# Kernel optimization log

Hardware: AMD Instinct MI355X
Metric: run time of the kernel (lower is better)

The kernel has to match this reference:

```python
import jax, jax.numpy as jnp
import numpy as np

NEG_SLOPE = 0.2


def setup_inputs() -> dict:
    key = jax.random.key(0)
    ks = jax.random.split(key, 8)
    N, E, FIN, H, D, C = 50000, 1000000, 128, 4, 32, 16
    feat = jax.random.normal(ks[0], (N, FIN), dtype=jnp.float32)
    y = jax.random.normal(ks[1], (N, C), dtype=jnp.float32)
    src = jax.random.randint(ks[2], (E,), 0, N, dtype=jnp.int32)
    dst = jax.random.randint(ks[3], (E,), 0, N, dtype=jnp.int32)
    fc_w = jax.random.normal(ks[4], (FIN, H * D), dtype=jnp.float32) * 0.05
    attn_l = jax.random.normal(ks[5], (H, D), dtype=jnp.float32) * 0.1
    attn_r = jax.random.normal(ks[6], (H, D), dtype=jnp.float32) * 0.1
    bias = jnp.zeros((H * D,), dtype=jnp.float32)
    return dict(feat=feat, y=y, fc_w=fc_w, attn_l=attn_l, attn_r=attn_r,
                bias=bias, src=src, dst=dst)


def reference(feat, y, fc_w, attn_l, attn_r, bias, src, dst):
    N = feat.shape[0]
    H, D = attn_l.shape
    # shared projection (feat_src == feat_dst for a homogeneous graph)
    ft = (feat @ fc_w).reshape(N, H, D)            # (N, H, D)
    el = jnp.sum(ft * attn_l[None], axis=-1)       # (N, H)
    er = jnp.sum(ft * attn_r[None], axis=-1)       # (N, H)
    # per-edge score: e_ij = leaky_relu(el[src] + er[dst])
    e = jax.nn.leaky_relu(el[src] + er[dst], negative_slope=NEG_SLOPE)  # (E, H)
    # segment softmax over edges grouped by destination node
    m = jax.ops.segment_max(e, dst, num_segments=N)                     # (N, H)
    m = jnp.where(jnp.isfinite(m), m, jnp.zeros_like(m))                # empty segments
    ee = jnp.exp(e - m[dst])                                            # (E, H)
    s = jax.ops.segment_sum(ee, dst, num_segments=N)                    # (N, H)
    a = ee / jnp.maximum(s[dst], 1e-9)                                  # (E, H)
    # scatter-aggregate weighted messages
    msg = ft[src] * a[:, :, None]                                       # (E, H, D)
    rst = jax.ops.segment_sum(msg, dst, num_segments=N)                 # (N, H, D)
    rst = rst + bias.reshape(1, H, D)
    # propagate labels y with the same attention (broadcast (C,) * (H,1) -> (H,C))
    ymsg = y[src][:, None, :] * a[:, :, None]                           # (E, H, C)
    y_pred = jax.ops.segment_sum(ymsg, dst, num_segments=N)             # (N, H, C)
    return rst, y_pred
```

## Files before the change

kernel.cpp:

```cpp
#include <hip/hip_runtime.h>
#include <hip/hip_bf16.h>

#define NEG_SLOPE 0.2f
#define ROWB 320
#define BSLOT 96
#define NSUBMAX 256
#define QCAP2 64
#define SUBSHIFT 8
#define SUBCAP 6400

typedef unsigned short u16;
typedef unsigned int u32;
typedef unsigned long long u64;

__device__ __forceinline__ u16 f32_to_bf16(float x) {
    u32 u = __float_as_uint(x);
    u32 r = u + 0x7fffu + ((u >> 16) & 1u);
    return (u16)(r >> 16);
}
__device__ __forceinline__ u32 bf16pair(float a, float b) {
    return (u32)f32_to_bf16(a) | ((u32)f32_to_bf16(b) << 16);
}
__device__ __forceinline__ float bflo(u32 u) { return __uint_as_float(u << 16); }
__device__ __forceinline__ float bfhi(u32 u) { return __uint_as_float(u & 0xffff0000u); }

__global__ __launch_bounds__(256) void k_binA2(
    const int* __restrict__ src, const int* __restrict__ dst,
    u32* __restrict__ subQ, int* __restrict__ subCursor, int nSub, int E) {
    __shared__ u32 q[NSUBMAX * QCAP2];
    __shared__ int lcnt[NSUBMAX], lbase[NSUBMAX];
    int t = threadIdx.x;
    lcnt[t] = 0;
    __syncthreads();
    int base = blockIdx.x * 4096;
#define PUSH(dd, sv)                                                      \
    {                                                                     \
        u32 bin_ = (u32)(dd) >> SUBSHIFT;                                 \
        u32 pair_ = ((u32)(dd) << 16) | ((u32)(sv) & 0xffffu);            \
        int p_ = atomicAdd(&lcnt[bin_], 1);                               \
        if (p_ < QCAP2) q[bin_ * QCAP2 + p_] = pair_;                     \
        else {                                                            \
            int gp_ = atomicAdd(&subCursor[bin_], 1);                     \
            if (gp_ < SUBCAP) subQ[(size_t)bin_ * SUBCAP + gp_] = pair_;  \
        }                                                                 \
    }
    for (int it = 0; it < 4; ++it) {
        int i = base + it * 1024 + t * 4;
        if (i + 4 <= E) {
            int4 d = *(const int4*)(dst + i);
            int4 s = *(const int4*)(src + i);
            PUSH(d.x, s.x); PUSH(d.y, s.y); PUSH(d.z, s.z); PUSH(d.w, s.w);
        } else {
            for (int k = 0; k < 4 && i + k < E; ++k) PUSH(dst[i + k], src[i + k]);
        }
    }
#undef PUSH
    __syncthreads();
    if (t < nSub) {
        int c = min(lcnt[t], QCAP2);
        lbase[t] = atomicAdd(&subCursor[t], c);
    }
    __syncthreads();
    int lane = t & 63, wv = t >> 6;
    for (int b = wv; b < nSub; b += 4) {
        int c = min(lcnt[b], QCAP2);
        if (lane < c) {
            int gp = lbase[b] + lane;
            if (gp < SUBCAP) subQ[(size_t)b * SUBCAP + gp] = q[b * QCAP2 + lane];
        }
    }
}

__global__ __launch_bounds__(256) void k_fused(
    const float* __restrict__ feat, const float* __restrict__ fc_w,
    const float* __restrict__ y, const float* __restrict__ attn_l,
    const float* __restrict__ attn_r, char* __restrict__ comb,
    const u32* __restrict__ subQ, const int* __restrict__ subCursor,
    int* __restrict__ cnt, u16* __restrict__ ss, int N, int nSub) {
    __shared__ u32 w_lds[128 * 64];
    __shared__ float f_lds[64 * 128];
    int t = threadIdx.x;

    if ((int)blockIdx.x < nSub) {
        int b = blockIdx.x;
        int* hist = (int*)w_lds;
        int* cur = hist + 256;
        hist[t] = 0;
        cur[t] = 0;
        __syncthreads();
        int n_b = min(subCursor[b], SUBCAP);
        const u32* qb = subQ + (size_t)b * SUBCAP;

        for (int i = t * 4; i < n_b; i += 1024) {
            if (i + 4 <= n_b) {
                uint4 p4 = *(const uint4*)(qb + i);
                atomicAdd(&hist[(p4.x >> 16) & 255], 1);
                atomicAdd(&hist[(p4.y >> 16) & 255], 1);
                atomicAdd(&hist[(p4.z >> 16) & 255], 1);
                atomicAdd(&hist[(p4.w >> 16) & 255], 1);
            } else {
                for (int k = i; k < n_b; ++k) atomicAdd(&hist[(qb[k] >> 16) & 255], 1);
            }
        }
        __syncthreads();
        int node = (b << SUBSHIFT) + t;
        if (node < N) cnt[node] = min(hist[t], BSLOT);

        for (int i = t * 4; i < n_b; i += 1024) {
            if (i + 4 <= n_b) {
                uint4 p4 = *(const uint4*)(qb + i);
                u32 pa[4] = {p4.x, p4.y, p4.z, p4.w};
#pragma unroll
                for (int k = 0; k < 4; ++k) {
                    int r = (pa[k] >> 16) & 255;
                    int p = atomicAdd(&cur[r], 1);
                    if (p < BSLOT)
                        ss[(size_t)(pa[k] >> 16) * BSLOT + p] = (u16)(pa[k] & 0xffffu);
                }
            } else {
                for (int k = i; k < n_b; ++k) {
                    u32 pr = qb[k];
                    int r = (pr >> 16) & 255;
                    int p = atomicAdd(&cur[r], 1);
                    if (p < BSLOT)
                        ss[(size_t)(pr >> 16) * BSLOT + p] = (u16)(pr & 0xffffu);
                }
            }
        }
        return;
    }

    int pb = (int)blockIdx.x - nSub;
    int n0 = pb * 64;
    if (pb == 0 && t < 80) {
        float* srow = (float*)(comb + (size_t)N * ROWB);
        srow[t] = (t >= 72 && t < 76) ? -1e30f : 0.f;
    }

#pragma unroll
    for (int it = 0; it < 16; ++it) {
        int i = it * 256 + t;
        float4 v = *(const float4*)(fc_w + 4 * i);
        int k = i >> 5, cp = 2 * (i & 31);
        *(uint2*)(w_lds + k * 64 + cp) = make_uint2(bf16pair(v.x, v.y), bf16pair(v.z, v.w));
    }
#pragma unroll
    for (int it = 0; it < 8; ++it) {
        int i = it * 256 + t;
        int n = i >> 5, q4 = 4 * (i & 31);
        float4 v = make_float4(0.f, 0.f, 0.f, 0.f);
        if (n0 + n < N) v = *(const float4*)(feat + (size_t)(n0 + n) * 128 + q4);
        *(float4*)(f_lds + n * 128 + q4) = v;
    }
#pragma unroll
    for (int it = 0; it < 4; ++it) {
        int i = it * 256 + t;
        int n = i >> 4, col = i & 15;
        if (n0 + n < N) {
            float yv = y[(size_t)(n0 + n) * 16 + col];
            *(u16*)(comb + (size_t)(n0 + n) * ROWB + 256 + 2 * col) = f32_to_bf16(yv);
        }
    }
    __syncthreads();

    int c = t & 31;
    int g = t >> 5;

    float acc[8][4];
#pragma unroll
    for (int j = 0; j < 8; ++j)
#pragma unroll
        for (int q = 0; q < 4; ++q) acc[j][q] = 0.f;

    const u32* wp = w_lds + 2 * c;
    const float* fp = f_lds + (8 * g) * 128;
    for (int k = 0; k < 128; k += 4) {
        uint2 wq0 = *(const uint2*)(wp + (k + 0) * 64);
        uint2 wq1 = *(const uint2*)(wp + (k + 1) * 64);
        uint2 wq2 = *(const uint2*)(wp + (k + 2) * 64);
        uint2 wq3 = *(const uint2*)(wp + (k + 3) * 64);
        float w00 = bflo(wq0.x), w01 = bfhi(wq0.x), w02 = bflo(wq0.y), w03 = bfhi(wq0.y);
        float w10 = bflo(wq1.x), w11 = bfhi(wq1.x), w12 = bflo(wq1.y), w13 = bfhi(wq1.y);
        float w20 = bflo(wq2.x), w21 = bfhi(wq2.x), w22 = bflo(wq2.y), w23 = bfhi(wq2.y);
        float w30 = bflo(wq3.x), w31 = bfhi(wq3.x), w32 = bflo(wq3.y), w33 = bfhi(wq3.y);
#pragma unroll
        for (int j = 0; j < 8; ++j) {
            float4 f = *(const float4*)(fp + j * 128 + k);
            acc[j][0] = fmaf(f.x, w00, acc[j][0]);
            acc[j][1] = fmaf(f.x, w01, acc[j][1]);
            acc[j][2] = fmaf(f.x, w02, acc[j][2]);
            acc[j][3] = fmaf(f.x, w03, acc[j][3]);
            acc[j][0] = fmaf(f.y, w10, acc[j][0]);
            acc[j][1] = fmaf(f.y, w11, acc[j][1]);
            acc[j][2] = fmaf(f.y, w12, acc[j][2]);
            acc[j][3] = fmaf(f.y, w13, acc[j][3]);
            acc[j][0] = fmaf(f.z, w20, acc[j][0]);
            acc[j][1] = fmaf(f.z, w21, acc[j][1]);
            acc[j][2] = fmaf(f.z, w22, acc[j][2]);
            acc[j][3] = fmaf(f.z, w23, acc[j][3]);
            acc[j][0] = fmaf(f.w, w30, acc[j][0]);
            acc[j][1] = fmaf(f.w, w31, acc[j][1]);
            acc[j][2] = fmaf(f.w, w32, acc[j][2]);
            acc[j][3] = fmaf(f.w, w33, acc[j][3]);
        }
    }

    float4 al4 = *(const float4*)(attn_l + 4 * c);
    float4 ar4 = *(const float4*)(attn_r + 4 * c);

#pragma unroll
    for (int j = 0; j < 8; ++j) {
        int n = n0 + 8 * g + j;
        bool ok = n < N;
        char* row = comb + (size_t)n * ROWB;
        if (ok) {
            *(uint2*)(row + 8 * c) =
                make_uint2(bf16pair(acc[j][0], acc[j][1]), bf16pair(acc[j][2], acc[j][3]));
        }
        float p = acc[j][0] * al4.x + acc[j][1] * al4.y + acc[j][2] * al4.z + acc[j][3] * al4.w;
        float q = acc[j][0] * ar4.x + acc[j][1] * ar4.y + acc[j][2] * ar4.z + acc[j][3] * ar4.w;
#pragma unroll
        for (int off = 1; off < 8; off <<= 1) {
            p += __shfl_xor(p, off);
            q += __shfl_xor(q, off);
        }
        if (ok && (c & 7) == 0) {
            float* ep = (float*)(row + 288);
            ep[c >> 3] = p;
            ep[4 + (c >> 3)] = q;
        }
    }
}

__global__ __launch_bounds__(256) void k_agg(
    const char* __restrict__ comb, const float* __restrict__ bias,
    const int* __restrict__ cnt, const u16* __restrict__ ss,
    float* __restrict__ rst, float* __restrict__ yp, int N) {
    __shared__ float ee_lds[4][256];
    int w = (int)((blockIdx.x * (size_t)blockDim.x + threadIdx.x) >> 6);
    int lane = threadIdx.x & 63;
    int wv = threadIdx.x >> 6;
    if (w >= N) return;

    int sub = lane & 31;
    int p = lane >> 5;
    bool isft = sub < 16;
    bool isy = (sub >= 16) && (sub < 24);
    int head = isft ? (sub >> 2) : (isy ? ((sub - 16) >> 1) : 0);
    int voff = isft ? 16 * sub : (256 + 16 * ((sub - 16) & 1));

    const char* roww = comb + (size_t)w * ROWB;
    float4 er4 = *(const float4*)(roww + 304);

    int deg = min(cnt[w], BSLOT);
    int degp = min((deg + 7) & ~7, BSLOT);
    int beg = w * BSLOT;

    float acc0 = 0.f, acc1 = 0.f, acc2 = 0.f, acc3 = 0.f;
    float acc4 = 0.f, acc5 = 0.f, acc6 = 0.f, acc7 = 0.f;
    float ssum = 0.f;
    float* my_ee = &ee_lds[wv][0];
    const float* eeL = my_ee + 4 * p + head;

#define LOADS(qq, V, Ee)                                        \
    {                                                           \
        int s0_ = __builtin_amdgcn_readlane(my_s, 2 * (qq));    \
        int s1_ = __builtin_amdgcn_readlane(my_s, 2 * (qq) + 1);\
        int s_ = p ? s1_ : s0_;                                 \
        const char* rb_ = comb + (size_t)s_ * ROWB;             \
        V = *(const uint4*)(rb_ + voff);                        \
        Ee = eeL[8 * (qq)];                                     \
    }
#define COMPS(V, Ee)                                            \
    {                                                           \
        ssum += Ee;                                             \
        acc0 = fmaf(Ee, bflo(V.x), acc0);                       \
        acc1 = fmaf(Ee, bfhi(V.x), acc1);                       \
        acc2 = fmaf(Ee, bflo(V.y), acc2);                       \
        acc3 = fmaf(Ee, bfhi(V.y), acc3);                       \
        acc4 = fmaf(Ee, bflo(V.z), acc4);                       \
        acc5 = fmaf(Ee, bfhi(V.z), acc5);                       \
        acc6 = fmaf(Ee, bflo(V.w), acc6);                       \
        acc7 = fmaf(Ee, bfhi(V.w), acc7);                       \
    }
#define LOAD4A(gg)                                              \
    {                                                           \
        int b4_ = 4 * (gg);                                     \
        LOADS(b4_ + 0, va0, ea0); LOADS(b4_ + 1, va1, ea1);     \
        LOADS(b4_ + 2, va2, ea2); LOADS(b4_ + 3, va3, ea3);     \
    }
#define LOAD4B(gg)                                              \
    {                                                           \
        int b4_ = 4 * (gg);                                     \
        LOADS(b4_ + 0, vb0, eb0); LOADS(b4_ + 1, vb1, eb1);     \
        LOADS(b4_ + 2, vb2, eb2); LOADS(b4_ + 3, vb3, eb3);     \
    }
#define COMP4A { COMPS(va0, ea0); COMPS(va1, ea1); COMPS(va2, ea2); COMPS(va3, ea3); }
#define COMP4B { COMPS(vb0, eb0); COMPS(vb1, eb1); COMPS(vb2, eb2); COMPS(vb3, eb3); }

    for (int off = 0; off < degp; off += 64) {
        int cl = min(64, degp - off);
        int my_s = (int)ss[beg + off + lane];
        my_s = (off + lane < deg) ? my_s : N;

        {
            const float4 el4 = *(const float4*)(comb + (size_t)my_s * ROWB + 288);
            float4 e4;
            e4.x = el4.x + er4.x;
            e4.y = el4.y + er4.y;
            e4.z = el4.z + er4.z;
            e4.w = el4.w + er4.w;
            float4 ee4;
            ee4.x = __expf(fmaxf(e4.x, NEG_SLOPE * e4.x));
            ee4.y = __expf(fmaxf(e4.y, NEG_SLOPE * e4.y));
            ee4.z = __expf(fmaxf(e4.z, NEG_SLOPE * e4.z));
            ee4.w = __expf(fmaxf(e4.w, NEG_SLOPE * e4.w));
            *(float4*)(my_ee + 4 * lane) = ee4;
        }

        int ngr = cl >> 3;
        uint4 va0, va1, va2, va3, vb0, vb1, vb2, vb3;
        float ea0, ea1, ea2, ea3, eb0, eb1, eb2, eb3;

        LOAD4A(0);
        int q = 0;
        for (; q + 2 <= ngr; q += 2) {
            LOAD4B(q + 1);
            COMP4A;
            if (q + 2 < ngr) LOAD4A(q + 2);
            COMP4B;
        }
        if (q < ngr) COMP4A;
    }
#undef LOADS
#undef COMPS
#undef LOAD4A
#undef LOAD4B
#undef COMP4A
#undef COMP4B

    ssum += __shfl_xor(ssum, 32);
    acc0 += __shfl_xor(acc0, 32);
    acc1 += __shfl_xor(acc1, 32);
    acc2 += __shfl_xor(acc2, 32);
    acc3 += __shfl_xor(acc3, 32);
    acc4 += __shfl_xor(acc4, 32);
    acc5 += __shfl_xor(acc5, 32);
    acc6 += __shfl_xor(acc6, 32);
    acc7 += __shfl_xor(acc7, 32);

    float inv = 1.f / fmaxf(ssum, 1e-9f);
    if (p == 0) {
        if (isft) {
            float4 b0 = *(const float4*)(bias + 8 * sub);
            float4 b1 = *(const float4*)(bias + 8 * sub + 4);
            float4 o0 = make_float4(fmaf(acc0, inv, b0.x), fmaf(acc1, inv, b0.y),
                                    fmaf(acc2, inv, b0.z), fmaf(acc3, inv, b0.w));
            float4 o1 = make_float4(fmaf(acc4, inv, b1.x), fmaf(acc5, inv, b1.y),
                                    fmaf(acc6, inv, b1.z), fmaf(acc7, inv, b1.w));
            *(float4*)(rst + (size_t)w * 128 + 8 * sub) = o0;
            *(float4*)(rst + (size_t)w * 128 + 8 * sub + 4) = o1;
        } else if (isy) {
            int yi = sub - 16;
            int hh = yi >> 1, hf = yi & 1;
            float4 o0 = make_float4(acc0 * inv, acc1 * inv, acc2 * inv, acc3 * inv);
            float4 o1 = make_float4(acc4 * inv, acc5 * inv, acc6 * inv, acc7 * inv);
            *(float4*)(yp + (size_t)w * 64 + 16 * hh + 8 * hf) = o0;
            *(float4*)(yp + (size_t)w * 64 + 16 * hh + 8 * hf + 4) = o1;
        }
    }
}

extern "C" void kernel_launch(void* const* d_in, const int* in_sizes, int n_in,
                              void* d_out, int out_size, void* d_ws, size_t ws_size,
                              hipStream_t stream) {
    const float* feat   = (const float*)d_in[0];
    const float* y      = (const float*)d_in[1];
    const float* fc_w   = (const float*)d_in[2];
    const float* attn_l = (const float*)d_in[3];
    const float* attn_r = (const float*)d_in[4];
    const float* bias   = (const float*)d_in[5];
    const int*   src    = (const int*)d_in[6];
    const int*   dst    = (const int*)d_in[7];

    const int N = in_sizes[0] / 128;
    const int E = in_sizes[6];

    char* comb = (char*)d_ws;
    int* cnt = (int*)(comb + (size_t)(N + 1) * ROWB);
    int* subCursor = cnt + N;
    u16* ss = (u16*)(subCursor + NSUBMAX);
    u32* subQ = (u32*)(ss + (size_t)BSLOT * N);

    float* rst = (float*)d_out;
    float* yp = rst + (size_t)N * 128;

    const int nSub = (N + 255) >> SUBSHIFT;
    const int projB = (N + 63) / 64;
    const int binAB = (E + 4095) / 4096;

    (void)hipMemsetAsync(subCursor, 0, NSUBMAX * sizeof(int), stream);
    k_binA2<<<dim3(binAB), dim3(256), 0, stream>>>(
        src, dst, subQ, subCursor, nSub, E);
    k_fused<<<dim3(nSub + projB), dim3(256), 0, stream>>>(
        feat, fc_w, y, attn_l, attn_r, comb, subQ, subCursor, cnt, ss, N, nSub);
    k_agg<<<dim3(((size_t)N * 64 + 255) / 256), dim3(256), 0, stream>>>(
        comb, bias, cnt, ss, rst, yp, N);
}
```

Measured before the change: 120.4 us.

## Fuse edge binning with projection and move per-node bucketing into separate kernel

The first binning pass (edge to sub-bin queues) now runs inside the same launch as the feature projection, reusing the projection's shared-memory buffers as the per-bin staging queue. The second pass (per-node histogram and slot scatter) moves out of the fused kernel into its own kernel. The aim is to overlap the atomic-heavy binning with the compute-bound projection instead of running binning alone. The cost is a heavier block mix in one launch and an extra launch for the per-node pass.

New measurement: 123.6 us. +2.7%, slower.

```diff
diff --git a/kernel.cpp b/kernel.cpp
--- a/kernel.cpp
+++ b/kernel.cpp
@@ -24,113 +24,67 @@
 __device__ __forceinline__ float bflo(u32 u) { return __uint_as_float(u << 16); }
 __device__ __forceinline__ float bfhi(u32 u) { return __uint_as_float(u & 0xffff0000u); }
 
-__global__ __launch_bounds__(256) void k_binA2(
-    const int* __restrict__ src, const int* __restrict__ dst,
-    u32* __restrict__ subQ, int* __restrict__ subCursor, int nSub, int E) {
-    __shared__ u32 q[NSUBMAX * QCAP2];
-    __shared__ int lcnt[NSUBMAX], lbase[NSUBMAX];
-    int t = threadIdx.x;
-    lcnt[t] = 0;
-    __syncthreads();
-    int base = blockIdx.x * 4096;
-#define PUSH(dd, sv)                                                      \
-    {                                                                     \
-        u32 bin_ = (u32)(dd) >> SUBSHIFT;                                 \
-        u32 pair_ = ((u32)(dd) << 16) | ((u32)(sv) & 0xffffu);            \
-        int p_ = atomicAdd(&lcnt[bin_], 1);                               \
-        if (p_ < QCAP2) q[bin_ * QCAP2 + p_] = pair_;                     \
-        else {                                                            \
-            int gp_ = atomicAdd(&subCursor[bin_], 1);                     \
-            if (gp_ < SUBCAP) subQ[(size_t)bin_ * SUBCAP + gp_] = pair_;  \
-        }                                                                 \
-    }
-    for (int it = 0; it < 4; ++it) {
-        int i = base + it * 1024 + t * 4;
-        if (i + 4 <= E) {
-            int4 d = *(const int4*)(dst + i);
-            int4 s = *(const int4*)(src + i);
-            PUSH(d.x, s.x); PUSH(d.y, s.y); PUSH(d.z, s.z); PUSH(d.w, s.w);
-        } else {
-            for (int k = 0; k < 4 && i + k < E; ++k) PUSH(dst[i + k], src[i + k]);
-        }
-    }
-#undef PUSH
-    __syncthreads();
-    if (t < nSub) {
-        int c = min(lcnt[t], QCAP2);
-        lbase[t] = atomicAdd(&subCursor[t], c);
-    }
-    __syncthreads();
-    int lane = t & 63, wv = t >> 6;
-    for (int b = wv; b < nSub; b += 4) {
-        int c = min(lcnt[b], QCAP2);
-        if (lane < c) {
-            int gp = lbase[b] + lane;
-            if (gp < SUBCAP) subQ[(size_t)b * SUBCAP + gp] = q[b * QCAP2 + lane];
-        }
-    }
-}
-
-__global__ __launch_bounds__(256) void k_fused(
+__global__ __launch_bounds__(256) void k_f1(
     const float* __restrict__ feat, const float* __restrict__ fc_w,
     const float* __restrict__ y, const float* __restrict__ attn_l,
     const float* __restrict__ attn_r, char* __restrict__ comb,
-    const u32* __restrict__ subQ, const int* __restrict__ subCursor,
-    int* __restrict__ cnt, u16* __restrict__ ss, int N, int nSub) {
+    const int* __restrict__ src, const int* __restrict__ dst,
+    u32* __restrict__ subQ, int* __restrict__ subCursor,
+    int N, int E, int nSub, int binAB) {
     __shared__ u32 w_lds[128 * 64];
     __shared__ float f_lds[64 * 128];
+    __shared__ int aux[512];
     int t = threadIdx.x;
 
-    if ((int)blockIdx.x < nSub) {
-        int b = blockIdx.x;
-        int* hist = (int*)w_lds;
-        int* cur = hist + 256;
-        hist[t] = 0;
-        cur[t] = 0;
+    if ((int)blockIdx.x < binAB) {
+        int* lcnt = aux;
+        int* lbase = aux + 256;
+        lcnt[t] = 0;
         __syncthreads();
-        int n_b = min(subCursor[b], SUBCAP);
-        const u32* qb = subQ + (size_t)b * SUBCAP;
-
-        for (int i = t * 4; i < n_b; i += 1024) {
-            if (i + 4 <= n_b) {
-                uint4 p4 = *(const uint4*)(qb + i);
-                atomicAdd(&hist[(p4.x >> 16) & 255], 1);
-                atomicAdd(&hist[(p4.y >> 16) & 255], 1);
-                atomicAdd(&hist[(p4.z >> 16) & 255], 1);
-                atomicAdd(&hist[(p4.w >> 16) & 255], 1);
+        int base = blockIdx.x * 4096;
+#define PUSH(dd, sv)                                                      \
+        {                                                                 \
+            u32 bin_ = (u32)(dd) >> SUBSHIFT;                             \
+            u32 pair_ = ((u32)(dd) << 16) | ((u32)(sv) & 0xffffu);        \
+            int p_ = atomicAdd(&lcnt[bin_], 1);                           \
+            if (p_ < QCAP2) {                                             \
+                u32* q_ = (bin_ & 128u) ? (u32*)f_lds : w_lds;            \
+                q_[(bin_ & 127u) * QCAP2 + p_] = pair_;                   \
+            } else {                                                      \
+                int gp_ = atomicAdd(&subCursor[bin_], 1);                 \
+                if (gp_ < SUBCAP) subQ[(size_t)bin_ * SUBCAP + gp_] = pair_; \
+            }                                                             \
+        }
+        for (int it = 0; it < 4; ++it) {
+            int i = base + it * 1024 + t * 4;
+            if (i + 4 <= E) {
+                int4 d = *(const int4*)(dst + i);
+                int4 s = *(const int4*)(src + i);
+                PUSH(d.x, s.x); PUSH(d.y, s.y); PUSH(d.z, s.z); PUSH(d.w, s.w);
             } else {
-                for (int k = i; k < n_b; ++k) atomicAdd(&hist[(qb[k] >> 16) & 255], 1);
+                for (int k = 0; k < 4 && i + k < E; ++k) PUSH(dst[i + k], src[i + k]);
             }
         }
+#undef PUSH
         __syncthreads();
-        int node = (b << SUBSHIFT) + t;
-        if (node < N) cnt[node] = min(hist[t], BSLOT);
-
-        for (int i = t * 4; i < n_b; i += 1024) {
-            if (i + 4 <= n_b) {
-                uint4 p4 = *(const uint4*)(qb + i);
-                u32 pa[4] = {p4.x, p4.y, p4.z, p4.w};
-#pragma unroll
-                for (int k = 0; k < 4; ++k) {
-                    int r = (pa[k] >> 16) & 255;
-                    int p = atomicAdd(&cur[r], 1);
-                    if (p < BSLOT)
-                        ss[(size_t)(pa[k] >> 16) * BSLOT + p] = (u16)(pa[k] & 0xffffu);
-                }
-            } else {
-                for (int k = i; k < n_b; ++k) {
-                    u32 pr = qb[k];
-                    int r = (pr >> 16) & 255;
-                    int p = atomicAdd(&cur[r], 1);
-                    if (p < BSLOT)
-                        ss[(size_t)(pr >> 16) * BSLOT + p] = (u16)(pr & 0xffffu);
-                }
+        if (t < nSub) {
+            int c = min(lcnt[t], QCAP2);
+            lbase[t] = atomicAdd(&subCursor[t], c);
+        }
+        __syncthreads();
+        int lane = t & 63, wv = t >> 6;
+        for (int b = wv; b < nSub; b += 4) {
+            int c = min(lcnt[b], QCAP2);
+            if (lane < c) {
+                int gp = lbase[b] + lane;
+                const u32* q_ = (b & 128) ? (const u32*)f_lds : w_lds;
+                if (gp < SUBCAP) subQ[(size_t)b * SUBCAP + gp] = q_[(b & 127) * QCAP2 + lane];
             }
         }
         return;
     }
 
-    int pb = (int)blockIdx.x - nSub;
+    int pb = (int)blockIdx.x - binAB;
     int n0 = pb * 64;
     if (pb == 0 && t < 80) {
         float* srow = (float*)(comb + (size_t)N * ROWB);
@@ -232,6 +186,57 @@
     }
 }
 
+__global__ __launch_bounds__(256) void k_passC(
+    const u32* __restrict__ subQ, const int* __restrict__ subCursor,
+    int* __restrict__ cnt, u16* __restrict__ ss, int N) {
+    __shared__ int hist[256];
+    __shared__ int cur[256];
+    int t = threadIdx.x;
+    int b = blockIdx.x;
+    hist[t] = 0;
+    cur[t] = 0;
+    __syncthreads();
+    int n_b = min(subCursor[b], SUBCAP);
+    const u32* qb = subQ + (size_t)b * SUBCAP;
+
+    for (int i = t * 4; i < n_b; i += 1024) {
+        if (i + 4 <= n_b) {
+            uint4 p4 = *(const uint4*)(qb + i);
+            atomicAdd(&hist[(p4.x >> 16) & 255], 1);
+            atomicAdd(&hist[(p4.y >> 16) & 255], 1);
+            atomicAdd(&hist[(p4.z >> 16) & 255], 1);
+            atomicAdd(&hist[(p4.w >> 16) & 255], 1);
+        } else {
+            for (int k = i; k < n_b; ++k) atomicAdd(&hist[(qb[k] >> 16) & 255], 1);
+        }
+    }
+    __syncthreads();
+    int node = (b << SUBSHIFT) + t;
+    if (node < N) cnt[node] = min(hist[t], BSLOT);
+
+    for (int i = t * 4; i < n_b; i += 1024) {
+        if (i + 4 <= n_b) {
+            uint4 p4 = *(const uint4*)(qb + i);
+            u32 pa[4] = {p4.x, p4.y, p4.z, p4.w};
+#pragma unroll
+            for (int k = 0; k < 4; ++k) {
+                int r = (pa[k] >> 16) & 255;
+                int p = atomicAdd(&cur[r], 1);
+                if (p < BSLOT)
+                    ss[(size_t)(pa[k] >> 16) * BSLOT + p] = (u16)(pa[k] & 0xffffu);
+            }
+        } else {
+            for (int k = i; k < n_b; ++k) {
+                u32 pr = qb[k];
+                int r = (pr >> 16) & 255;
+                int p = atomicAdd(&cur[r], 1);
+                if (p < BSLOT)
+                    ss[(size_t)(pr >> 16) * BSLOT + p] = (u16)(pr & 0xffffu);
+            }
+        }
+    }
+}
+
 __global__ __launch_bounds__(256) void k_agg(
     const char* __restrict__ comb, const float* __restrict__ bias,
     const int* __restrict__ cnt, const u16* __restrict__ ss,
@@ -400,10 +405,10 @@
     const int binAB = (E + 4095) / 4096;
 
     (void)hipMemsetAsync(subCursor, 0, NSUBMAX * sizeof(int), stream);
-    k_binA2<<<dim3(binAB), dim3(256), 0, stream>>>(
-        src, dst, subQ, subCursor, nSub, E);
-    k_fused<<<dim3(nSub + projB), dim3(256), 0, stream>>>(
-        feat, fc_w, y, attn_l, attn_r, comb, subQ, subCursor, cnt, ss, N, nSub);
+    k_f1<<<dim3(binAB + projB), dim3(256), 0, stream>>>(
+        feat, fc_w, y, attn_l, attn_r, comb, src, dst, subQ, subCursor,
+        N, E, nSub, binAB);
+    k_passC<<<dim3(nSub), dim3(256), 0, stream>>>(subQ, subCursor, cnt, ss, N);
     k_agg<<<dim3(((size_t)N * 64 + 255) / 256), dim3(256), 0, stream>>>(
         comb, bias, cnt, ss, rst, yp, N);
 }
```

## Compute node projection GEMM with bf16 MFMA instead of scalar FMAs

Applied to the files above, without the earlier changes.

Replaces the scalar-FMA feat@fc_w projection in the fused kernel with __builtin_amdgcn_mfma_f32_16x16x32_bf16. Weights and features are staged in LDS as bf16 in an MFMA-friendly layout, with padded feature rows to reduce bank conflicts. Results go back through LDS so the existing epilogue can compute el/er and write rows. This adds an extra LDS round trip and barrier, and el/er are now computed from bf16-rounded features, a small precision change.

Result: faster. 109.0 us (median of 3 runs) (-9.5%).

```diff
diff --git a/kernel.cpp b/kernel.cpp
--- a/kernel.cpp
+++ b/kernel.cpp
@@ -12,6 +12,8 @@
 typedef unsigned short u16;
 typedef unsigned int u32;
 typedef unsigned long long u64;
+typedef __attribute__((ext_vector_type(8))) short bf16x8;
+typedef __attribute__((ext_vector_type(4))) float f32x4;
 
 __device__ __forceinline__ u16 f32_to_bf16(float x) {
     u32 u = __float_as_uint(x);
@@ -77,14 +79,14 @@
     const float* __restrict__ attn_r, char* __restrict__ comb,
     const u32* __restrict__ subQ, const int* __restrict__ subCursor,
     int* __restrict__ cnt, u16* __restrict__ ss, int N, int nSub) {
-    __shared__ u32 w_lds[128 * 64];
-    __shared__ float f_lds[64 * 128];
+    __shared__ u16 w16[16384];
+    __shared__ u16 f16[64 * 136];
+    __shared__ int hist[256];
+    __shared__ int cur[256];
     int t = threadIdx.x;
 
     if ((int)blockIdx.x < nSub) {
         int b = blockIdx.x;
-        int* hist = (int*)w_lds;
-        int* cur = hist + 256;
         hist[t] = 0;
         cur[t] = 0;
         __syncthreads();
@@ -141,16 +143,22 @@
     for (int it = 0; it < 16; ++it) {
         int i = it * 256 + t;
         float4 v = *(const float4*)(fc_w + 4 * i);
-        int k = i >> 5, cp = 2 * (i & 31);
-        *(uint2*)(w_lds + k * 64 + cp) = make_uint2(bf16pair(v.x, v.y), bf16pair(v.z, v.w));
+        int k = i >> 5, jq = i & 31;
+        int kt = k >> 5, h2 = (k >> 3) & 3, i0 = k & 7;
+        int jt = jq >> 2, jm0 = (jq & 3) * 4;
+        int base = ((jt * 4 + kt) * 64 + 16 * h2 + jm0) * 8 + i0;
+        w16[base] = f32_to_bf16(v.x);
+        w16[base + 8] = f32_to_bf16(v.y);
+        w16[base + 16] = f32_to_bf16(v.z);
+        w16[base + 24] = f32_to_bf16(v.w);
     }
 #pragma unroll
     for (int it = 0; it < 8; ++it) {
         int i = it * 256 + t;
-        int n = i >> 5, q4 = 4 * (i & 31);
+        int n = i >> 5, q4 = (i & 31) * 4;
         float4 v = make_float4(0.f, 0.f, 0.f, 0.f);
         if (n0 + n < N) v = *(const float4*)(feat + (size_t)(n0 + n) * 128 + q4);
-        *(float4*)(f_lds + n * 128 + q4) = v;
+        *(uint2*)(f16 + n * 136 + q4) = make_uint2(bf16pair(v.x, v.y), bf16pair(v.z, v.w));
     }
 #pragma unroll
     for (int it = 0; it < 4; ++it) {
@@ -163,48 +171,35 @@
     }
     __syncthreads();
 
+    int wv2 = t >> 6, l = t & 63;
+    int m = l & 15, h = l >> 4;
+
+    f32x4 acc[8];
+#pragma unroll
+    for (int jt = 0; jt < 8; ++jt) acc[jt] = (f32x4){0.f, 0.f, 0.f, 0.f};
+
+    const u16* arow = f16 + (16 * wv2 + m) * 136 + 8 * h;
+#pragma unroll
+    for (int kt = 0; kt < 4; ++kt) {
+        uint4 av = *(const uint4*)(arow + kt * 32);
+        bf16x8 a = __builtin_bit_cast(bf16x8, av);
+#pragma unroll
+        for (int jt = 0; jt < 8; ++jt) {
+            uint4 bv = *(const uint4*)(w16 + ((jt * 4 + kt) * 64 + l) * 8);
+            bf16x8 bfr = __builtin_bit_cast(bf16x8, bv);
+            acc[jt] = __builtin_amdgcn_mfma_f32_16x16x32_bf16(a, bfr, acc[jt], 0, 0, 0);
+        }
+    }
+
+#pragma unroll
+    for (int jt = 0; jt < 8; ++jt)
+#pragma unroll
+        for (int r = 0; r < 4; ++r)
+            f16[(16 * wv2 + 4 * h + r) * 136 + 16 * jt + m] = f32_to_bf16(acc[jt][r]);
+    __syncthreads();
+
     int c = t & 31;
     int g = t >> 5;
-
-    float acc[8][4];
-#pragma unroll
-    for (int j = 0; j < 8; ++j)
-#pragma unroll
-        for (int q = 0; q < 4; ++q) acc[j][q] = 0.f;
-
-    const u32* wp = w_lds + 2 * c;
-    const float* fp = f_lds + (8 * g) * 128;
-    for (int k = 0; k < 128; k += 4) {
-        uint2 wq0 = *(const uint2*)(wp + (k + 0) * 64);
-        uint2 wq1 = *(const uint2*)(wp + (k + 1) * 64);
-        uint2 wq2 = *(const uint2*)(wp + (k + 2) * 64);
-        uint2 wq3 = *(const uint2*)(wp + (k + 3) * 64);
-        float w00 = bflo(wq0.x), w01 = bfhi(wq0.x), w02 = bflo(wq0.y), w03 = bfhi(wq0.y);
-        float w10 = bflo(wq1.x), w11 = bfhi(wq1.x), w12 = bflo(wq1.y), w13 = bfhi(wq1.y);
-        float w20 = bflo(wq2.x), w21 = bfhi(wq2.x), w22 = bflo(wq2.y), w23 = bfhi(wq2.y);
-        float w30 = bflo(wq3.x), w31 = bfhi(wq3.x), w32 = bflo(wq3.y), w33 = bfhi(wq3.y);
-#pragma unroll
-        for (int j = 0; j < 8; ++j) {
-            float4 f = *(const float4*)(fp + j * 128 + k);
-            acc[j][0] = fmaf(f.x, w00, acc[j][0]);
-            acc[j][1] = fmaf(f.x, w01, acc[j][1]);
-            acc[j][2] = fmaf(f.x, w02, acc[j][2]);
-            acc[j][3] = fmaf(f.x, w03, acc[j][3]);
-            acc[j][0] = fmaf(f.y, w10, acc[j][0]);
-            acc[j][1] = fmaf(f.y, w11, acc[j][1]);
-            acc[j][2] = fmaf(f.y, w12, acc[j][2]);
-            acc[j][3] = fmaf(f.y, w13, acc[j][3]);
-            acc[j][0] = fmaf(f.z, w20, acc[j][0]);
-            acc[j][1] = fmaf(f.z, w21, acc[j][1]);
-            acc[j][2] = fmaf(f.z, w22, acc[j][2]);
-            acc[j][3] = fmaf(f.z, w23, acc[j][3]);
-            acc[j][0] = fmaf(f.w, w30, acc[j][0]);
-            acc[j][1] = fmaf(f.w, w31, acc[j][1]);
-            acc[j][2] = fmaf(f.w, w32, acc[j][2]);
-            acc[j][3] = fmaf(f.w, w33, acc[j][3]);
-        }
-    }
-
     float4 al4 = *(const float4*)(attn_l + 4 * c);
     float4 ar4 = *(const float4*)(attn_r + 4 * c);
 
@@ -212,13 +207,12 @@
     for (int j = 0; j < 8; ++j) {
         int n = n0 + 8 * g + j;
         bool ok = n < N;
+        uint2 cv = *(const uint2*)(f16 + (8 * g + j) * 136 + 4 * c);
+        float f0 = bflo(cv.x), f1 = bfhi(cv.x), f2 = bflo(cv.y), f3 = bfhi(cv.y);
         char* row = comb + (size_t)n * ROWB;
-        if (ok) {
-            *(uint2*)(row + 8 * c) =
-                make_uint2(bf16pair(acc[j][0], acc[j][1]), bf16pair(acc[j][2], acc[j][3]));
-        }
-        float p = acc[j][0] * al4.x + acc[j][1] * al4.y + acc[j][2] * al4.z + acc[j][3] * al4.w;
-        float q = acc[j][0] * ar4.x + acc[j][1] * ar4.y + acc[j][2] * ar4.z + acc[j][3] * ar4.w;
+        if (ok) *(uint2*)(row + 8 * c) = cv;
+        float p = f0 * al4.x + f1 * al4.y + f2 * al4.z + f3 * al4.w;
+        float q = f0 * ar4.x + f1 * ar4.y + f2 * ar4.z + f3 * ar4.w;
 #pragma unroll
         for (int off = 1; off < 8; off <<= 1) {
             p += __shfl_xor(p, off);
```
